# Performance work log

Hardware: AMD Instinct MI355X
Metric: run time of the kernel (lower is better)

The kernel has to match this reference:

```python
import jax, jax.numpy as jnp
import numpy as np

N = 8192
D_IN = 1024
D_OUT = 1024


def setup_inputs() -> dict:
    key = jax.random.key(0)
    ks = jax.random.split(key, 7)
    s = 1.0 / np.sqrt(D_IN)
    return {
        "feat": jax.random.normal(ks[0], (N, D_IN), dtype=jnp.float32),
        "Wq": jax.random.uniform(ks[1], (D_IN, D_OUT), jnp.float32, -s, s),
        "bq": jax.random.uniform(ks[2], (D_OUT,), jnp.float32, -s, s),
        "Wk": jax.random.uniform(ks[3], (D_IN, D_OUT), jnp.float32, -s, s),
        "bk": jax.random.uniform(ks[4], (D_OUT,), jnp.float32, -s, s),
        "Wv": jax.random.uniform(ks[5], (D_IN, D_OUT), jnp.float32, -s, s),
        "bv": jax.random.uniform(ks[6], (D_OUT,), jnp.float32, -s, s),
    }


def reference(feat, Wq, bq, Wk, bk, Wv, bv):
    # eval mode: dropout(p=0.3, training=False) is identity
    q = feat @ Wq + bq          # [N, D_OUT]
    k = feat @ Wk + bk          # [N, D_OUT]
    v = feat @ Wv + bv          # [N, D_OUT]
    scale = 1.0 / jnp.sqrt(jnp.float32(D_OUT))
    scores = (q @ k.T) * scale  # [N, N]
    attn = jax.nn.softmax(scores, axis=1)
    return attn @ v             # [N, D_OUT]
```

## Files before the change

kernel.cpp:

```cpp
#include <hip/hip_runtime.h>
#include <hip/hip_bf16.h>
#include <stdint.h>

typedef __hip_bfloat16 bf16;
typedef __attribute__((ext_vector_type(8))) short short8;
typedef __attribute__((ext_vector_type(4))) float f32x4;

#define BM 128
#define BN 128

__device__ __forceinline__ unsigned short f2bf_bits(float x) {
    return __builtin_bit_cast(unsigned short, __float2bfloat16(x));
}

__device__ __forceinline__ void gload_lds16(const bf16* g, bf16* l) {
    __builtin_amdgcn_global_load_lds(
        (const __attribute__((address_space(1))) void*)(const void*)g,
        (__attribute__((address_space(3))) void*)(void*)l,
        16, 0, 0);
}

__global__ void prep_kernel(const float* __restrict__ feat, unsigned short* __restrict__ featb,
                            const float* __restrict__ W0, const float* __restrict__ W1,
                            const float* __restrict__ W2, bf16* __restrict__ Wt,
                            float* __restrict__ lsum) {
    const int b = blockIdx.x;
    const int tid = threadIdx.x;
    if (b < 8192) {
        int i = b * 256 + tid;
        float4 v = reinterpret_cast<const float4*>(feat)[i];
        ushort4 o;
        o.x = f2bf_bits(v.x); o.y = f2bf_bits(v.y);
        o.z = f2bf_bits(v.z); o.w = f2bf_bits(v.w);
        reinterpret_cast<ushort4*>(featb)[i] = o;
    } else if (b < 11264) {
        __shared__ float tile[32][33];
        const int b2 = b - 8192;
        const int z = b2 >> 10;
        const int t = b2 & 1023;
        const int bx = t & 31, by = t >> 5;
        const int tx = tid & 31, ty = tid >> 5;
        const float* in = (z == 0) ? W0 : (z == 1) ? W1 : W2;
        bf16* out = Wt + (size_t)z * 1024 * 1024;
        for (int r = ty; r < 32; r += 8)
            tile[r][tx] = in[(size_t)(by * 32 + r) * 1024 + bx * 32 + tx];
        __syncthreads();
        for (int r = ty; r < 32; r += 8)
            out[(size_t)(bx * 32 + r) * 1024 + by * 32 + tx] = __float2bfloat16(tile[tx][r]);
    } else {
        for (int i = tid; i < 8192; i += 256) lsum[i] = 0.f;
    }
}

__global__ void scale_rows(float* __restrict__ out, const float* __restrict__ lsum) {
    int i = blockIdx.x * 256 + threadIdx.x;
    float4 v = reinterpret_cast<float4*>(out)[i];
    float inv = 1.0f / lsum[i >> 8];
    v.x *= inv; v.y *= inv; v.z *= inv; v.w *= inv;
    reinterpret_cast<float4*>(out)[i] = v;
}

template <int MODE, int KH, int SWAP>
__global__ __launch_bounds__(256, 4)
void gemm_bt(const bf16* __restrict__ A, const bf16* __restrict__ B,
             const float* __restrict__ b0, const float* __restrict__ b1,
             const float* __restrict__ b2, float* __restrict__ lsum,
             bf16* __restrict__ outb, float* __restrict__ outf,
             int M, int N, int K, int ldb, int ldout, float scale) {
    constexpr int TILE = 128 * 32;
    constexpr int SELEMS = (2 * KH * TILE < 9216) ? 9216 : 2 * KH * TILE;
    __shared__ bf16 smem[SELEMS];
    bf16* As = smem;
    bf16* Bs = smem + KH * TILE;

    const int tid  = threadIdx.x;
    const int lane = tid & 63;
    const int wave = tid >> 6;
    const int wm = wave & 1, wn = wave >> 1;
    const int l16  = lane & 15;
    const int quad = lane >> 4;
    long bm0, bn0;
    if (SWAP == 2) {
        const int lin = blockIdx.y * 8 + blockIdx.x;
        const int xcd = lin & 7;
        const int s   = lin >> 3;
        bn0 = (long)(s & 7) * BN;
        bm0 = (long)((s >> 3) * 8 + xcd) * BM;
    } else {
        bm0 = (long)(SWAP ? blockIdx.y : blockIdx.x) * BM;
        bn0 = (long)(SWAP ? blockIdx.x : blockIdx.y) * BN;
    }

    const float* bias = nullptr;
    if (MODE == 0) {
        const int z = blockIdx.z;
        B    += (size_t)z * N * K;
        outb += (size_t)z * M * ldout;
        bias  = (z == 0) ? b0 : b1;
    }

    const int lrow = lane >> 2;
    const int lcol = (lane & 3) * 8;
    const bf16* gA[2][KH];
    const bf16* gB[2][KH];
    bf16* lA[2][KH];
    bf16* lB[2][KH];
#pragma unroll
    for (int u = 0; u < 2; u++)
#pragma unroll
        for (int h = 0; h < KH; h++) {
            gA[u][h] = A + (size_t)(bm0 + wave * 32 + u * 16 + lrow) * K + h * 32 + lcol;
            gB[u][h] = B + (size_t)(bn0 + wave * 32 + u * 16 + lrow) * ldb + h * 32 + lcol;
            lA[u][h] = As + h * TILE + (wave * 32 + u * 16) * 32;
            lB[u][h] = Bs + h * TILE + (wave * 32 + u * 16) * 32;
        }

    const bf16* Ard = As + (wm * 64 + l16) * 32 + quad * 8;
    const bf16* Brd = Bs + (wn * 64 + l16) * 32 + quad * 8;

    f32x4 acc[4][4];
    const f32x4 zero = {0.f, 0.f, 0.f, 0.f};
#pragma unroll
    for (int i = 0; i < 4; i++)
#pragma unroll
        for (int j = 0; j < 4; j++) acc[i][j] = zero;

    for (int k0 = 0; k0 < K; k0 += KH * 32) {
        __syncthreads();
#pragma unroll
        for (int u = 0; u < 2; u++)
#pragma unroll
            for (int h = 0; h < KH; h++) {
                gload_lds16(gA[u][h] + k0, lA[u][h]);
                gload_lds16(gB[u][h] + k0, lB[u][h]);
            }
        __syncthreads();
#pragma unroll
        for (int h = 0; h < KH; h++) {
            short8 af[4], bfr[4];
#pragma unroll
            for (int mi = 0; mi < 4; mi++)
                af[mi] = *reinterpret_cast<const short8*>(Ard + h * TILE + mi * 16 * 32);
#pragma unroll
            for (int ni = 0; ni < 4; ni++)
                bfr[ni] = *reinterpret_cast<const short8*>(Brd + h * TILE + ni * 16 * 32);
#pragma unroll
            for (int mi = 0; mi < 4; mi++)
#pragma unroll
                for (int ni = 0; ni < 4; ni++)
                    acc[mi][ni] = __builtin_amdgcn_mfma_f32_16x16x32_bf16(af[mi], bfr[ni], acc[mi][ni], 0, 0, 0);
        }
    }

    if (MODE == 0 || MODE == 1 || MODE == 5) {
        __syncthreads();
        bf16* eb = smem + wave * 1152;
        float bcol[4];
        if (MODE == 0) {
#pragma unroll
            for (int ni = 0; ni < 4; ni++) bcol[ni] = bias[bn0 + wn * 64 + l16 + ni * 16];
        }
#pragma unroll
        for (int mi = 0; mi < 4; mi++) {
#pragma unroll
            for (int r = 0; r < 4; r++) {
                float s = 0.f;
                float brow = 0.f;
                if (MODE == 5) brow = b2[bm0 + wm * 64 + mi * 16 + quad * 4 + r];
#pragma unroll
                for (int ni = 0; ni < 4; ni++) {
                    float v = acc[mi][ni][r];
                    if (MODE == 0)      v += bcol[ni];
                    else if (MODE == 5) v += brow;
                    else { v = __expf(v * scale); s += v; }
                    eb[(quad * 4 + r) * 72 + ni * 16 + l16] = __float2bfloat16(v);
                }
                if (MODE == 1) {
                    s += __shfl_xor(s, 1);
                    s += __shfl_xor(s, 2);
                    s += __shfl_xor(s, 4);
                    s += __shfl_xor(s, 8);
                    if (l16 == 0) atomicAdd(&lsum[bm0 + wm * 64 + mi * 16 + quad * 4 + r], s);
                }
            }
            asm volatile("s_waitcnt lgkmcnt(0)" ::: "memory");
#pragma unroll
            for (int p = 0; p < 2; p++) {
                int r2 = p * 8 + (lane >> 3);
                int c2 = (lane & 7) * 8;
                short8 val = *reinterpret_cast<const short8*>(eb + r2 * 72 + c2);
                *reinterpret_cast<short8*>(
                    outb + (size_t)(bm0 + wm * 64 + mi * 16 + r2) * ldout + bn0 + wn * 64 + c2) = val;
            }
            asm volatile("s_waitcnt lgkmcnt(0)" ::: "memory");
        }
    } else {
        const int rb2 = wm * 64 + quad * 4;
        const int cb2 = wn * 64 + l16;
#pragma unroll
        for (int mi = 0; mi < 4; mi++)
#pragma unroll
            for (int r = 0; r < 4; r++) {
                long row = bm0 + rb2 + mi * 16 + r;
                float mul = (MODE == 3) ? 1.0f / lsum[row] : 0.f;
#pragma unroll
                for (int ni = 0; ni < 4; ni++) {
                    long col = bn0 + cb2 + ni * 16;
                    if (MODE == 3) outf[row * ldout + col] = acc[mi][ni][r] * mul;
                    else           outf[row * ldout + col] += acc[mi][ni][r];
                }
            }
    }
}

extern "C" void kernel_launch(void* const* d_in, const int* in_sizes, int n_in,
                              void* d_out, int out_size, void* d_ws, size_t ws_size,
                              hipStream_t stream) {
    const float* feat = (const float*)d_in[0];
    const float* Wq   = (const float*)d_in[1];
    const float* bqv  = (const float*)d_in[2];
    const float* Wk   = (const float*)d_in[3];
    const float* bkv  = (const float*)d_in[4];
    const float* Wv   = (const float*)d_in[5];
    const float* bvv  = (const float*)d_in[6];
    float* outp = (float*)d_out;

    const int M = 8192, D = 1024;
    char* ws = (char*)d_ws;
    size_t off = 0;
    auto carve = [&](size_t bytes) -> char* {
        char* r = ws + off;
        off += (bytes + 255) & ~(size_t)255;
        return r;
    };
    bf16* featb = (bf16*)carve((size_t)M * D * 2);
    bf16* Wbt   = (bf16*)carve((size_t)3 * D * D * 2);
    bf16* qk    = (bf16*)carve((size_t)2 * M * D * 2);
    bf16* vbt   = (bf16*)carve((size_t)D * M * 2);
    float* lsum = (float*)carve((size_t)M * 4);
    size_t avail = (ws_size > off) ? ws_size - off : 0;

    int C;
    if      (avail >= (size_t)M * M * 2)    C = M;
    else if (avail >= (size_t)M * 4096 * 2) C = 4096;
    else if (avail >= (size_t)M * 2048 * 2) C = 2048;
    else                                    C = 1024;
    bf16* Pc = (bf16*)carve((size_t)M * C * 2);

    prep_kernel<<<dim3(11265), dim3(256), 0, stream>>>(
        feat, (unsigned short*)featb, Wq, Wk, Wv, Wbt, lsum);
    gemm_bt<0, 2, 0><<<dim3(M / 128, D / 128, 2), dim3(256), 0, stream>>>(
        featb, Wbt, bqv, bkv, nullptr, nullptr, qk, nullptr, M, D, D, D, D, 1.0f);
    gemm_bt<5, 2, 0><<<dim3(D / 128, M / 128), dim3(256), 0, stream>>>(
        Wbt + (size_t)2 * D * D, featb, nullptr, nullptr, bvv, nullptr, vbt, nullptr,
        D, M, D, D, M, 1.0f);

    const float scale = 0.03125f;
    bf16* qb = qk;
    bf16* kb = qk + (size_t)M * D;
    if (C == M) {
        gemm_bt<1, 2, 0><<<dim3(M / 128, M / 128), dim3(256), 0, stream>>>(
            qb, kb, nullptr, nullptr, nullptr, lsum, Pc, nullptr, M, M, D, D, M, scale);
        gemm_bt<3, 2, 2><<<dim3(D / 128, M / 128), dim3(256), 0, stream>>>(
            Pc, vbt, nullptr, nullptr, nullptr, lsum, nullptr, outp, M, D, M, M, D, 0.f);
    } else {
        hipMemsetAsync(outp, 0, (size_t)M * D * 4, stream);
        for (int c = 0; c < M / C; c++) {
            gemm_bt<1, 2, 0><<<dim3(M / 128, C / 128), dim3(256), 0, stream>>>(
                qb, kb + (size_t)c * C * D, nullptr, nullptr, nullptr, lsum, Pc, nullptr,
                M, C, D, D, C, scale);
            gemm_bt<2, 2, 1><<<dim3(D / 128, M / 128), dim3(256), 0, stream>>>(
                Pc, vbt + (size_t)c * C, nullptr, nullptr, nullptr, nullptr, nullptr, outp,
                M, D, C, M, D, 0.f);
        }
        scale_rows<<<dim3(M * D / 4 / 256), dim3(256), 0, stream>>>(outp, lsum);
    }
}
```

Measured before the change: 445.9 us.

## Merge V-transpose projection into the QK projection launch via third grid slice

The separate MODE 5 launch that computed V transposed is folded into the MODE 0 QKV projection as a third blockIdx.z slice, which swaps the A/B operands and writes with leading dimension M into a contiguous buffer after q and k. The epilogue staging buffer now alternates between two LDS regions per mi iteration, so the trailing lgkmcnt wait after each store can be removed. This saves one kernel launch and lets the V tiles share a grid with the Q/K tiles for better occupancy. It relies on the z==2 slice's swapped indexing (blockIdx.y used as the M tile and blockIdx.x as the N tile) matching the V shape, and on LDS having room for the doubled staging buffers.

```diff
diff --git a/kernel.cpp b/kernel.cpp
--- a/kernel.cpp
+++ b/kernel.cpp
@@ -91,12 +91,24 @@
         bn0 = (long)(SWAP ? blockIdx.x : blockIdx.y) * BN;
     }
 
-    const float* bias = nullptr;
+    const bf16* Ause = A;
+    const bf16* Buse = B;
+    bf16* oz = outb;
+    int  ldo = ldout;
+    int  z   = 0;
     if (MODE == 0) {
-        const int z = blockIdx.z;
-        B    += (size_t)z * N * K;
-        outb += (size_t)z * M * ldout;
-        bias  = (z == 0) ? b0 : b1;
+        z = blockIdx.z;
+        if (z == 2) {
+            bm0  = (long)blockIdx.y * BM;
+            bn0  = (long)blockIdx.x * BN;
+            Ause = B + (size_t)2 * N * K;
+            Buse = A;
+            oz   = outb + (size_t)2 * M * ldout;
+            ldo  = M;
+        } else {
+            Buse = B + (size_t)z * N * K;
+            oz   = outb + (size_t)z * M * ldout;
+        }
     }
 
     const int lrow = lane >> 2;
@@ -109,8 +121,8 @@
     for (int u = 0; u < 2; u++)
 #pragma unroll
         for (int h = 0; h < KH; h++) {
-            gA[u][h] = A + (size_t)(bm0 + wave * 32 + u * 16 + lrow) * K + h * 32 + lcol;
-            gB[u][h] = B + (size_t)(bn0 + wave * 32 + u * 16 + lrow) * ldb + h * 32 + lcol;
+            gA[u][h] = Ause + (size_t)(bm0 + wave * 32 + u * 16 + lrow) * K + h * 32 + lcol;
+            gB[u][h] = Buse + (size_t)(bn0 + wave * 32 + u * 16 + lrow) * ldb + h * 32 + lcol;
             lA[u][h] = As + h * TILE + (wave * 32 + u * 16) * 32;
             lB[u][h] = Bs + h * TILE + (wave * 32 + u * 16) * 32;
         }
@@ -152,26 +164,26 @@
         }
     }
 
-    if (MODE == 0 || MODE == 1 || MODE == 5) {
-        __syncthreads();
-        bf16* eb = smem + wave * 1152;
+    if (MODE == 0 || MODE == 1) {
+        __syncthreads();
         float bcol[4];
-        if (MODE == 0) {
+        if (MODE == 0 && z < 2) {
+            const float* bias = (z == 0) ? b0 : b1;
 #pragma unroll
             for (int ni = 0; ni < 4; ni++) bcol[ni] = bias[bn0 + wn * 64 + l16 + ni * 16];
         }
 #pragma unroll
         for (int mi = 0; mi < 4; mi++) {
+            bf16* eb = smem + ((wave << 1) | (mi & 1)) * 1152;
 #pragma unroll
             for (int r = 0; r < 4; r++) {
                 float s = 0.f;
                 float brow = 0.f;
-                if (MODE == 5) brow = b2[bm0 + wm * 64 + mi * 16 + quad * 4 + r];
+                if (MODE == 0 && z == 2) brow = b2[bm0 + wm * 64 + mi * 16 + quad * 4 + r];
 #pragma unroll
                 for (int ni = 0; ni < 4; ni++) {
                     float v = acc[mi][ni][r];
-                    if (MODE == 0)      v += bcol[ni];
-                    else if (MODE == 5) v += brow;
+                    if (MODE == 0) v += (z == 2) ? brow : bcol[ni];
                     else { v = __expf(v * scale); s += v; }
                     eb[(quad * 4 + r) * 72 + ni * 16 + l16] = __float2bfloat16(v);
                 }
@@ -190,9 +202,8 @@
                 int c2 = (lane & 7) * 8;
                 short8 val = *reinterpret_cast<const short8*>(eb + r2 * 72 + c2);
                 *reinterpret_cast<short8*>(
-                    outb + (size_t)(bm0 + wm * 64 + mi * 16 + r2) * ldout + bn0 + wn * 64 + c2) = val;
-            }
-            asm volatile("s_waitcnt lgkmcnt(0)" ::: "memory");
+                    oz + (size_t)(bm0 + wm * 64 + mi * 16 + r2) * ldo + bn0 + wn * 64 + c2) = val;
+            }
         }
     } else {
         const int rb2 = wm * 64 + quad * 4;
@@ -235,8 +246,8 @@
     };
     bf16* featb = (bf16*)carve((size_t)M * D * 2);
     bf16* Wbt   = (bf16*)carve((size_t)3 * D * D * 2);
-    bf16* qk    = (bf16*)carve((size_t)2 * M * D * 2);
-    bf16* vbt   = (bf16*)carve((size_t)D * M * 2);
+    bf16* qk    = (bf16*)carve((size_t)2 * M * D * 2 + (size_t)D * M * 2);
+    bf16* vbt   = qk + (size_t)2 * M * D;
     float* lsum = (float*)carve((size_t)M * 4);
     size_t avail = (ws_size > off) ? ws_size - off : 0;
 
@@ -249,11 +260,8 @@
 
     prep_kernel<<<dim3(11265), dim3(256), 0, stream>>>(
         feat, (unsigned short*)featb, Wq, Wk, Wv, Wbt, lsum);
-    gemm_bt<0, 2, 0><<<dim3(M / 128, D / 128, 2), dim3(256), 0, stream>>>(
-        featb, Wbt, bqv, bkv, nullptr, nullptr, qk, nullptr, M, D, D, D, D, 1.0f);
-    gemm_bt<5, 2, 0><<<dim3(D / 128, M / 128), dim3(256), 0, stream>>>(
-        Wbt + (size_t)2 * D * D, featb, nullptr, nullptr, bvv, nullptr, vbt, nullptr,
-        D, M, D, D, M, 1.0f);
+    gemm_bt<0, 2, 0><<<dim3(M / 128, D / 128, 3), dim3(256), 0, stream>>>(
+        featb, Wbt, bqv, bkv, bvv, nullptr, qk, nullptr, M, D, D, D, D, 1.0f);
 
     const float scale = 0.03125f;
     bf16* qb = qk;
```

Measured after the change: 439.4 us. About the same (-1.5%).
